# Kernel tuning notes

Measured on AMD Instinct MI355X. Metric: run time of the kernel, lower is better.

## Reference

```python
import jax, jax.numpy as jnp
import numpy as np

B, N, D = 128, 512, 512
C = D // 2
K = 4            # topk from init
NUM_SAMPLES = 500
SIGMA = 0.05
NOISE_KEY = jax.random.key(12345)


def perturbed_topk(scores):
    # scores: (B, N) -> indicators (B, K, N)
    b, d = scores.shape
    noise = jax.random.normal(NOISE_KEY, (b, NUM_SAMPLES, d), dtype=scores.dtype)
    perturbed = scores[:, None, :] + noise * SIGMA        # (B, S, N)
    _, idx = jax.lax.top_k(perturbed, K)                  # (B, S, K)
    idx = jnp.sort(idx, axis=-1)
    onehot = jax.nn.one_hot(idx, d, dtype=jnp.float32)    # (B, S, K, N)
    return onehot.mean(axis=1)                            # (B, K, N)


def layer_norm(x, w, b, eps=1e-5):
    mu = x.mean(-1, keepdims=True)
    var = ((x - mu) ** 2).mean(-1, keepdims=True)
    return (x - mu) * jax.lax.rsqrt(var + eps) * w + b


def setup_inputs() -> dict:
    key = jax.random.key(0)
    ks = jax.random.split(key, 8)
    s = lambda fan_in: 1.0 / np.sqrt(fan_in)
    return {
        "x": jax.random.normal(ks[0], (B, N, D), dtype=jnp.float32),
        "input_ids": jax.random.randint(ks[1], (B, N), 0, 30000).astype(jnp.int64),
        "attention_mask": jnp.ones((B, N), dtype=jnp.float32),
        "ln_w": jnp.ones((D,), dtype=jnp.float32),
        "ln_b": jnp.zeros((D,), dtype=jnp.float32),
        "w1": jax.random.uniform(ks[2], (D, C), minval=-s(D), maxval=s(D)),
        "b1": jax.random.uniform(ks[3], (C,), minval=-s(D), maxval=s(D)),
        "w2": jax.random.uniform(ks[4], (D, C), minval=-s(D), maxval=s(D)),
        "w3": jax.random.uniform(ks[5], (C, 1), minval=-s(C), maxval=s(C)),
    }


def reference(x, input_ids, attention_mask, ln_w, ln_b, w1, b1, w2, w3):
    b, n, d = x.shape
    # TextPredictorLG.in_conv: LayerNorm -> Linear(D, D//2) -> GELU (exact erf)
    h = jax.nn.gelu(layer_norm(x, ln_w, ln_b) @ w1 + b1, approximate=False)  # (B,N,C)
    cls_pos = jnp.argmax(input_ids, axis=-1)                                 # (B,)
    g = h[jnp.arange(b), cls_pos][:, None, :]                                # (B,1,C)
    cat = jnp.concatenate([h, jnp.broadcast_to(g, (b, n, C))], axis=-1)      # (B,N,D)
    # out_conv: Linear(D, C, no bias) -> GELU -> Linear(C, 1, no bias) -> Sigmoid
    pred_score = jax.nn.sigmoid(jax.nn.gelu(cat @ w2, approximate=False) @ w3)[..., 0]  # (B,N)
    # shift attention mask left by one, zero-pad last position
    mask_new = jnp.concatenate(
        [attention_mask[:, 1:], jnp.zeros((b, 1), dtype=attention_mask.dtype)], axis=1)
    word_score = pred_score * mask_new                                       # (B,N)
    topk_indicator = perturbed_topk(word_score)                              # (B,K,N)
    cls_x = x[jnp.arange(b), cls_pos][:, None, :]                            # (B,1,D)
    selected = jnp.einsum('bkl,bld->bkd', topk_indicator, x)                 # (B,K,D)
    return jnp.concatenate([cls_x, selected], axis=1)                        # (B,1+K,D)
```

## Files before the change

### kernel.cpp

```cpp
#include <hip/hip_runtime.h>
#include <stdint.h>

#define T_B 128
#define T_N 512
#define T_D 512
#define T_C 256
#define T_S 500
#define T_K 4

#define OFF_HP       0ull
#define OFF_W1HT     67108864ull
#define OFF_W1LT     67371008ull
#define OFF_W2HT     67633152ull
#define OFF_W2LT     67764224ull
#define OFF_ROWSTAT  67895296ull
#define OFF_U        68419584ull
#define OFF_V        68420608ull
#define OFF_GTERM    68421632ull
#define OFF_SCORE    68552704ull
#define OFF_CLSPOS   68814848ull
#define OFF_COUNTS   0ull

typedef __attribute__((ext_vector_type(8))) short bf16x8;
typedef __attribute__((ext_vector_type(4))) float f32x4;

union BF8 { uint32_t u[4]; bf16x8 v; };

__device__ __forceinline__ float gelu_exact(float z) {
  return 0.5f * z * (1.0f + erff(z * 0.70710678118654752440f));
}

__device__ __forceinline__ uint32_t rne_bf16(float f) {
  uint32_t u = __float_as_uint(f);
  return (u + 0x7FFFu + ((u >> 16) & 1u)) >> 16;
}

__device__ __forceinline__ uint2 threefry2x32(uint32_t x0, uint32_t x1) {
  const uint32_t k0 = 0u;
  const uint32_t k1 = 12345u;
  const uint32_t k2 = k0 ^ k1 ^ 0x1BD11BDAu;
  x0 += k0; x1 += k1;
#define TF_ROUND(r) { x0 += x1; x1 = (x1 << (r)) | (x1 >> (32 - (r))); x1 ^= x0; }
  TF_ROUND(13) TF_ROUND(15) TF_ROUND(26) TF_ROUND(6)
  x0 += k1; x1 += k2 + 1u;
  TF_ROUND(17) TF_ROUND(29) TF_ROUND(16) TF_ROUND(24)
  x0 += k2; x1 += k0 + 2u;
  TF_ROUND(13) TF_ROUND(15) TF_ROUND(26) TF_ROUND(6)
  x0 += k0; x1 += k1 + 3u;
  TF_ROUND(17) TF_ROUND(29) TF_ROUND(16) TF_ROUND(24)
  x0 += k1; x1 += k2 + 4u;
  TF_ROUND(13) TF_ROUND(15) TF_ROUND(26) TF_ROUND(6)
  x0 += k2; x1 += k0 + 5u;
#undef TF_ROUND
  return make_uint2(x0, x1);
}

__device__ __forceinline__ float bits_to_u(uint32_t bits) {
  float f = __uint_as_float((bits >> 9) | 0x3F800000u) - 1.0f;
  float u = f * 2.0f - 0.99999994f;
  return fmaxf(-0.99999994f, u);
}

__device__ __forceinline__ float erfinv_f(float x) {
  float w = -log1pf(-x * x);
  float p;
  if (w < 5.0f) {
    w = w - 2.5f;
    p = 2.81022636e-08f;
    p = fmaf(p, w, 3.43273939e-07f);
    p = fmaf(p, w, -3.5233877e-06f);
    p = fmaf(p, w, -4.39150654e-06f);
    p = fmaf(p, w, 0.00021858087f);
    p = fmaf(p, w, -0.00125372503f);
    p = fmaf(p, w, -0.00417768164f);
    p = fmaf(p, w, 0.246640727f);
    p = fmaf(p, w, 1.50140941f);
  } else {
    w = sqrtf(w) - 3.0f;
    p = -0.000200214257f;
    p = fmaf(p, w, 0.000100950558f);
    p = fmaf(p, w, 0.00134934322f);
    p = fmaf(p, w, -0.00367342844f);
    p = fmaf(p, w, 0.00573950773f);
    p = fmaf(p, w, -0.0076224613f);
    p = fmaf(p, w, 0.00943887047f);
    p = fmaf(p, w, 1.00167406f);
    p = fmaf(p, w, 2.83297682f);
  }
  return p * x;
}

__device__ __forceinline__ void top4_wave(float v[8], const int lane, int idx[4]) {
#pragma unroll
  for (int it = 0; it < 4; it++) {
    float bv = -INFINITY;
    int bn = 0x7FFFFFFF;
#pragma unroll
    for (int j = 0; j < 8; j++) {
      const int n = (j << 6) + lane;
      const bool better = (v[j] > bv) || ((v[j] == bv) && (n < bn));
      bv = better ? v[j] : bv;
      bn = better ? n : bn;
    }
#pragma unroll
    for (int m = 32; m >= 1; m >>= 1) {
      const float ov = __shfl_xor(bv, m);
      const int   on = __shfl_xor(bn, m);
      const bool better = (ov > bv) || ((ov == bv) && (on < bn));
      bv = better ? ov : bv;
      bn = better ? on : bn;
    }
    idx[it] = bn;
    const int jj = bn >> 6;
    const bool own = (bn & 63) == lane;
#pragma unroll
    for (int j = 0; j < 8; j++)
      if (own && j == jj) v[j] = -INFINITY;
  }
}

__device__ __forceinline__ void sort4(int a[4]) {
#define CS(x, y) { int lo = min(a[x], a[y]); int hi = max(a[x], a[y]); a[x] = lo; a[y] = hi; }
  CS(0, 1) CS(2, 3) CS(0, 2) CS(1, 3) CS(1, 2)
#undef CS
}


__global__ __launch_bounds__(256) void rowstats_kernel(const float* __restrict__ x,
                                                       float2* __restrict__ rowstat) {
  const int lane = threadIdx.x & 63;
  const int row = blockIdx.x * 4 + (threadIdx.x >> 6);
  const float* xr = x + (size_t)row * 512;
  float vals[8];
  float s = 0.0f;
#pragma unroll
  for (int j = 0; j < 8; j++) { vals[j] = xr[j * 64 + lane]; s += vals[j]; }
#pragma unroll
  for (int m = 1; m < 64; m <<= 1) s += __shfl_xor(s, m);
  const float mu = s * (1.0f / 512.0f);
  float d2 = 0.0f;
#pragma unroll
  for (int j = 0; j < 8; j++) { float d = vals[j] - mu; d2 = fmaf(d, d, d2); }
#pragma unroll
  for (int m = 1; m < 64; m <<= 1) d2 += __shfl_xor(d2, m);
  const float var = d2 * (1.0f / 512.0f);
  if (lane == 0) rowstat[row] = make_float2(mu, rsqrtf(var + 1e-5f));
}

__global__ __launch_bounds__(256) void prep_kernel(const float* __restrict__ w1,
                                                   const float* __restrict__ lnw,
                                                   const float* __restrict__ w2,
                                                   ushort* __restrict__ w1hT,
                                                   ushort* __restrict__ w1lT,
                                                   ushort* __restrict__ w2hT,
                                                   ushort* __restrict__ w2lT) {
  const int c = blockIdx.x;
  const int t = threadIdx.x;
#pragma unroll
  for (int it = 0; it < 2; it++) {
    const int d = t + it * 256;
    const float f = lnw[d] * w1[d * 256 + c];
    const uint32_t hi = rne_bf16(f);
    const float lo = f - __uint_as_float(hi << 16);
    w1hT[c * 512 + d] = (ushort)hi;
    w1lT[c * 512 + d] = (ushort)rne_bf16(lo);
  }
  {
    const float f = w2[t * 256 + c];
    const uint32_t hi = rne_bf16(f);
    const float lo = f - __uint_as_float(hi << 16);
    w2hT[c * 256 + t] = (ushort)hi;
    w2lT[c * 256 + t] = (ushort)rne_bf16(lo);
  }
}

__global__ __launch_bounds__(256) void uv_kernel(const float* __restrict__ w1,
                                                 const float* __restrict__ lnw,
                                                 const float* __restrict__ lnb,
                                                 float* __restrict__ uvec,
                                                 float* __restrict__ vvec) {
  const int c = threadIdx.x;
  float u = 0.0f, v = 0.0f;
  for (int d = 0; d < 512; d++) {
    const float w = w1[d * 256 + c];
    u = fmaf(lnw[d], w, u);
    v = fmaf(lnb[d], w, v);
  }
  uvec[c] = u;
  vvec[c] = v;
}

__global__ __launch_bounds__(64) void clspos_kernel(const int* __restrict__ ids,
                                                    const float* __restrict__ x,
                                                    int* __restrict__ cls_pos,
                                                    float* __restrict__ out) {
  const int b = blockIdx.x;
  const int lane = threadIdx.x;
  unsigned long long best = 0ull;
#pragma unroll
  for (int j = 0; j < 8; j++) {
    const int n = j * 64 + lane;
    const unsigned v = (unsigned)ids[b * 512 + n];
    const unsigned long long key = ((unsigned long long)v << 32) | (unsigned)(511 - n);
    best = key > best ? key : best;
  }
#pragma unroll
  for (int m = 1; m < 64; m <<= 1) {
    const unsigned long long o = __shfl_xor(best, m);
    best = o > best ? o : best;
  }
  const int n = 511 - (int)(best & 0xFFFFFFFFu);
  if (lane == 0) cls_pos[b] = n;
  const float* xr = x + ((size_t)b * 512 + n) * 512;
  float* orow = out + (size_t)b * 2560;
#pragma unroll
  for (int j = 0; j < 8; j++) orow[j * 64 + lane] = xr[j * 64 + lane];
}

__global__ __launch_bounds__(256, 2) void gemm1_mfma(const float* __restrict__ x,
                                                     const ushort* __restrict__ w1hT,
                                                     const ushort* __restrict__ w1lT,
                                                     const float2* __restrict__ rowstat,
                                                     const float* __restrict__ uvec,
                                                     const float* __restrict__ vvec,
                                                     const float* __restrict__ b1,
                                                     uint32_t* __restrict__ Hp) {
  const int l = threadIdx.x & 63;
  const int wid = threadIdx.x >> 6;
  const int wm = wid >> 1, wn = wid & 1;
  const int lr = l & 15;
  const int g  = l >> 4;
  const int row0 = blockIdx.x * 128;

  f32x4 acc[4][8];
#pragma unroll
  for (int mt = 0; mt < 4; mt++)
#pragma unroll
    for (int nt = 0; nt < 8; nt++) acc[mt][nt] = (f32x4)0.0f;

  const float* xb = x + (size_t)(row0 + wm * 64 + lr) * 512 + g * 8;
  const ushort* bhb = w1hT + (size_t)(wn * 128 + lr) * 512 + g * 8;
  const ushort* blb = w1lT + (size_t)(wn * 128 + lr) * 512 + g * 8;

  for (int kt = 0; kt < 16; kt++) {
    const int ko = kt * 32;
    bf16x8 ah[4], al[4];
#pragma unroll
    for (int mt = 0; mt < 4; mt++) {
      const float4 f0 = *(const float4*)(xb + (size_t)mt * 16 * 512 + ko);
      const float4 f1 = *(const float4*)(xb + (size_t)mt * 16 * 512 + ko + 4);
      float f[8] = {f0.x, f0.y, f0.z, f0.w, f1.x, f1.y, f1.z, f1.w};
      BF8 H, L;
#pragma unroll
      for (int p = 0; p < 4; p++) {
        const uint32_t u0 = __float_as_uint(f[2 * p]);
        const uint32_t u1 = __float_as_uint(f[2 * p + 1]);
        H.u[p] = (u0 >> 16) | (u1 & 0xFFFF0000u);
        const float l0 = f[2 * p]     - __uint_as_float(u0 & 0xFFFF0000u);
        const float l1 = f[2 * p + 1] - __uint_as_float(u1 & 0xFFFF0000u);
        L.u[p] = rne_bf16(l0) | (rne_bf16(l1) << 16);
      }
      ah[mt] = H.v; al[mt] = L.v;
    }
#pragma unroll
    for (int nt = 0; nt < 8; nt++) {
      const bf16x8 bh = *(const bf16x8*)(bhb + (size_t)nt * 16 * 512 + ko);
      const bf16x8 bl = *(const bf16x8*)(blb + (size_t)nt * 16 * 512 + ko);
#pragma unroll
      for (int mt = 0; mt < 4; mt++) {
        acc[mt][nt] = __builtin_amdgcn_mfma_f32_16x16x32_bf16(ah[mt], bh, acc[mt][nt], 0, 0, 0);
        acc[mt][nt] = __builtin_amdgcn_mfma_f32_16x16x32_bf16(al[mt], bh, acc[mt][nt], 0, 0, 0);
        acc[mt][nt] = __builtin_amdgcn_mfma_f32_16x16x32_bf16(ah[mt], bl, acc[mt][nt], 0, 0, 0);
      }
    }
  }

#pragma unroll
  for (int mt = 0; mt < 4; mt++) {
    const int Rb = row0 + wm * 64 + mt * 16 + g * 4;
    float2 st[4];
#pragma unroll
    for (int r = 0; r < 4; r++) st[r] = rowstat[Rb + r];
#pragma unroll
    for (int nt = 0; nt < 8; nt++) {
      const int c = wn * 128 + nt * 16 + lr;
      const float uu = uvec[c];
      const float vvb = vvec[c] + b1[c];
      uint32_t pk[4];
#pragma unroll
      for (int r = 0; r < 4; r++) {
        const float z = st[r].y * (acc[mt][nt][r] - st[r].x * uu) + vvb;
        const float gg = gelu_exact(z);
        const uint32_t ug = __float_as_uint(gg);
        const uint32_t hi = ug >> 16;
        const float lo = gg - __uint_as_float(ug & 0xFFFF0000u);
        pk[r] = hi | (rne_bf16(lo) << 16);
      }
      uint32_t* dst = Hp + (size_t)(Rb >> 2) * 1024 + c * 4;
      *(uint4*)dst = make_uint4(pk[0], pk[1], pk[2], pk[3]);
    }
  }
}

__global__ __launch_bounds__(256) void gterm_kernel(const uint32_t* __restrict__ Hp,
                                                    const float* __restrict__ W2,
                                                    const int* __restrict__ cls_pos,
                                                    float* __restrict__ gterm) {
  __shared__ float gsh[256];
  const int b = blockIdx.x;
  const int t = threadIdx.x;
  const int r = b * 512 + cls_pos[b];
  const uint32_t u = Hp[(size_t)(r >> 2) * 1024 + t * 4 + (r & 3)];
  gsh[t] = __uint_as_float((u & 0xFFFFu) << 16) + __uint_as_float(u & 0xFFFF0000u);
  __syncthreads();
  float acc = 0.0f;
  for (int j = 0; j < 256; j++) acc = fmaf(gsh[j], W2[(256 + j) * 256 + t], acc);
  gterm[b * 256 + t] = acc;
}

__global__ __launch_bounds__(256, 2) void gemm2_mfma(const uint32_t* __restrict__ Hp,
                                                     const ushort* __restrict__ w2hT,
                                                     const ushort* __restrict__ w2lT,
                                                     const float* __restrict__ gterm,
                                                     const float* __restrict__ w3,
                                                     const float* __restrict__ amask,
                                                     float* __restrict__ score) {
  __shared__ float sbuf[128][2];
  const int l = threadIdx.x & 63;
  const int wid = threadIdx.x >> 6;
  const int wm = wid >> 1, wn = wid & 1;
  const int lr = l & 15;
  const int g  = l >> 4;
  const int row0 = blockIdx.x * 128;
  const int b = row0 >> 9;

  f32x4 acc[4][8];
#pragma unroll
  for (int mt = 0; mt < 4; mt++)
#pragma unroll
    for (int nt = 0; nt < 8; nt++) acc[mt][nt] = (f32x4)0.0f;

  const uint32_t* ab = Hp + (size_t)(((row0 + wm * 64) >> 2) + (lr >> 2)) * 1024 + (lr & 3) + g * 32;
  const ushort* bhb = w2hT + (size_t)(wn * 128 + lr) * 256 + g * 8;
  const ushort* blb = w2lT + (size_t)(wn * 128 + lr) * 256 + g * 8;

  for (int kt = 0; kt < 8; kt++) {
    const int ko = kt * 32;
    bf16x8 ah[4], al[4];
#pragma unroll
    for (int mt = 0; mt < 4; mt++) {
      const uint32_t* ap = ab + (size_t)mt * 4096 + kt * 128;
      uint32_t u[8];
#pragma unroll
      for (int j = 0; j < 8; j++) u[j] = ap[j * 4];
      BF8 H, L;
#pragma unroll
      for (int p = 0; p < 4; p++) {
        H.u[p] = (u[2 * p] & 0xFFFFu) | (u[2 * p + 1] << 16);
        L.u[p] = (u[2 * p] >> 16) | (u[2 * p + 1] & 0xFFFF0000u);
      }
      ah[mt] = H.v; al[mt] = L.v;
    }
#pragma unroll
    for (int nt = 0; nt < 8; nt++) {
      const bf16x8 bh = *(const bf16x8*)(bhb + (size_t)nt * 16 * 256 + ko);
      const bf16x8 bl = *(const bf16x8*)(blb + (size_t)nt * 16 * 256 + ko);
#pragma unroll
      for (int mt = 0; mt < 4; mt++) {
        acc[mt][nt] = __builtin_amdgcn_mfma_f32_16x16x32_bf16(ah[mt], bh, acc[mt][nt], 0, 0, 0);
        acc[mt][nt] = __builtin_amdgcn_mfma_f32_16x16x32_bf16(al[mt], bh, acc[mt][nt], 0, 0, 0);
        acc[mt][nt] = __builtin_amdgcn_mfma_f32_16x16x32_bf16(ah[mt], bl, acc[mt][nt], 0, 0, 0);
      }
    }
  }

  float s[4][4];
#pragma unroll
  for (int mt = 0; mt < 4; mt++)
#pragma unroll
    for (int r = 0; r < 4; r++) s[mt][r] = 0.0f;

#pragma unroll
  for (int nt = 0; nt < 8; nt++) {
    const int c = wn * 128 + nt * 16 + lr;
    const float gt = gterm[b * 256 + c];
    const float w3v = w3[c];
#pragma unroll
    for (int mt = 0; mt < 4; mt++)
#pragma unroll
      for (int r = 0; r < 4; r++)
        s[mt][r] = fmaf(gelu_exact(acc[mt][nt][r] + gt), w3v, s[mt][r]);
  }
#pragma unroll
  for (int mt = 0; mt < 4; mt++)
#pragma unroll
    for (int r = 0; r < 4; r++) {
#pragma unroll
      for (int m = 1; m < 16; m <<= 1) s[mt][r] += __shfl_xor(s[mt][r], m);
      if (lr == 0) sbuf[wm * 64 + mt * 16 + g * 4 + r][wn] = s[mt][r];
    }
  __syncthreads();
  const int t = threadIdx.x;
  if (t < 128) {
    const float ssum = sbuf[t][0] + sbuf[t][1];
    const int R = row0 + t;
    const int n = R & 511;
    const float mk = (n < 511) ? amask[(R >> 9) * 512 + n + 1] : 0.0f;
    score[R] = mk / (1.0f + expf(-ssum));
  }
}

__global__ __launch_bounds__(256) void topk_kernel(const float* __restrict__ score,
                                                   int* __restrict__ counts) {
  const int lane = threadIdx.x & 63;
  const int wid = threadIdx.x >> 6;
  const int p = blockIdx.x * 4 + wid;
  const int b = p / 500;
  const uint32_t ibase = (uint32_t)p * 512u;
  const float* sc = score + b * 512;

  float v[8];
#pragma unroll
  for (int j = 0; j < 8; j++) {
    const int n = (j << 6) + lane;
    const uint2 o = threefry2x32(0u, ibase + (uint32_t)n);
    const uint32_t bits = o.x ^ o.y;
    const float nz = 1.41421356f * erfinv_f(bits_to_u(bits));
    v[j] = sc[n] + nz * 0.05f;
  }
  int idx[4];
  top4_wave(v, lane, idx);
  sort4(idx);
  if (lane == 0) {
    const int base = b * (T_K * T_N);
#pragma unroll
    for (int k = 0; k < 4; k++)
      atomicAdd(&counts[base + k * 512 + idx[k]], 1);
  }
}

__global__ __launch_bounds__(256) void select_kernel(const int* __restrict__ counts,
                                                     const float* __restrict__ x,
                                                     float* __restrict__ out) {
  __shared__ float cnt[4][512];
  __shared__ int list[512];
  __shared__ int nlist;
  const int b = blockIdx.x;
  const int t = threadIdx.x;
  if (t == 0) nlist = 0;
  __syncthreads();
  for (int l = t; l < 512; l += 256) {
    const int base = b * 2048 + l;
    const int c0 = counts[base];
    const int c1 = counts[base + 512];
    const int c2 = counts[base + 1024];
    const int c3 = counts[base + 1536];
    cnt[0][l] = (float)c0 * (1.0f / 500.0f);
    cnt[1][l] = (float)c1 * (1.0f / 500.0f);
    cnt[2][l] = (float)c2 * (1.0f / 500.0f);
    cnt[3][l] = (float)c3 * (1.0f / 500.0f);
    if ((c0 | c1 | c2 | c3) != 0) {
      const int pos = atomicAdd(&nlist, 1);
      list[pos] = l;
    }
  }
  __syncthreads();
  const int L = nlist;
  float a0[4] = {0.f, 0.f, 0.f, 0.f};
  float a1[4] = {0.f, 0.f, 0.f, 0.f};
  for (int e = 0; e < L; e++) {
    const int l = list[e];
    const float x0 = x[((size_t)b * 512 + l) * 512 + t];
    const float x1 = x[((size_t)b * 512 + l) * 512 + t + 256];
#pragma unroll
    for (int k = 0; k < 4; k++) {
      const float c = cnt[k][l];
      a0[k] = fmaf(c, x0, a0[k]);
      a1[k] = fmaf(c, x1, a1[k]);
    }
  }
#pragma unroll
  for (int k = 0; k < 4; k++) {
    out[(size_t)b * 2560 + (k + 1) * 512 + t] = a0[k];
    out[(size_t)b * 2560 + (k + 1) * 512 + t + 256] = a1[k];
  }
}

extern "C" void kernel_launch(void* const* d_in, const int* in_sizes, int n_in,
                              void* d_out, int out_size, void* d_ws, size_t ws_size,
                              hipStream_t stream) {
  const float* x     = (const float*)d_in[0];
  const int*   ids   = (const int*)d_in[1];
  const float* amask = (const float*)d_in[2];
  const float* lnw   = (const float*)d_in[3];
  const float* lnb   = (const float*)d_in[4];
  const float* w1    = (const float*)d_in[5];
  const float* b1    = (const float*)d_in[6];
  const float* w2    = (const float*)d_in[7];
  const float* w3    = (const float*)d_in[8];
  float* out = (float*)d_out;
  char* ws = (char*)d_ws;

  uint32_t* Hp     = (uint32_t*)(ws + OFF_HP);
  ushort*   w1hT   = (ushort*)(ws + OFF_W1HT);
  ushort*   w1lT   = (ushort*)(ws + OFF_W1LT);
  ushort*   w2hT   = (ushort*)(ws + OFF_W2HT);
  ushort*   w2lT   = (ushort*)(ws + OFF_W2LT);
  float2*   rowstat= (float2*)(ws + OFF_ROWSTAT);
  float*    uvec   = (float*)(ws + OFF_U);
  float*    vvec   = (float*)(ws + OFF_V);
  float*    gterm  = (float*)(ws + OFF_GTERM);
  float*    score  = (float*)(ws + OFF_SCORE);
  int*      clspos = (int*)(ws + OFF_CLSPOS);
  int*      counts = (int*)(ws + OFF_COUNTS);

  rowstats_kernel<<<16384, 256, 0, stream>>>(x, rowstat);
  prep_kernel<<<256, 256, 0, stream>>>(w1, lnw, w2, w1hT, w1lT, w2hT, w2lT);
  uv_kernel<<<1, 256, 0, stream>>>(w1, lnw, lnb, uvec, vvec);
  clspos_kernel<<<128, 64, 0, stream>>>(ids, x, clspos, out);
  gemm1_mfma<<<512, 256, 0, stream>>>(x, w1hT, w1lT, rowstat, uvec, vvec, b1, Hp);
  gterm_kernel<<<128, 256, 0, stream>>>(Hp, w2, clspos, gterm);
  gemm2_mfma<<<512, 256, 0, stream>>>(Hp, w2hT, w2lT, gterm, w3, amask, score);
  hipMemsetAsync(counts, 0, 128 * 4 * 512 * sizeof(int), stream);
  topk_kernel<<<16000, 256, 0, stream>>>(score, counts);
  select_kernel<<<128, 256, 0, stream>>>(counts, x, out);
}
```

Before: 681.1 us.

## Halve GEMM row tiles for more blocks and streamline noisy top-k selection

Both MFMA GEMM kernels now process 64 rows per block instead of 128, with twice as many blocks and launch bounds raised to three blocks per CU. The aim is better occupancy and load balance on a GPU with many CUs, at the cost of reloading the weight tiles more often. The top-k kernel evaluates both erfinv branches without divergence, uses a fast log2 in place of log1pf, and packs each shifted positive float with its index into a 64-bit key so each wave reduction needs one shuffle instead of two. The faster log and the different rounding order could change which samples tie or cross, which would shift the top-k counts slightly.

```diff
diff --git a/kernel.cpp b/kernel.cpp
--- a/kernel.cpp
+++ b/kernel.cpp
@@ -55,70 +55,6 @@
   return make_uint2(x0, x1);
 }
 
-__device__ __forceinline__ float bits_to_u(uint32_t bits) {
-  float f = __uint_as_float((bits >> 9) | 0x3F800000u) - 1.0f;
-  float u = f * 2.0f - 0.99999994f;
-  return fmaxf(-0.99999994f, u);
-}
-
-__device__ __forceinline__ float erfinv_f(float x) {
-  float w = -log1pf(-x * x);
-  float p;
-  if (w < 5.0f) {
-    w = w - 2.5f;
-    p = 2.81022636e-08f;
-    p = fmaf(p, w, 3.43273939e-07f);
-    p = fmaf(p, w, -3.5233877e-06f);
-    p = fmaf(p, w, -4.39150654e-06f);
-    p = fmaf(p, w, 0.00021858087f);
-    p = fmaf(p, w, -0.00125372503f);
-    p = fmaf(p, w, -0.00417768164f);
-    p = fmaf(p, w, 0.246640727f);
-    p = fmaf(p, w, 1.50140941f);
-  } else {
-    w = sqrtf(w) - 3.0f;
-    p = -0.000200214257f;
-    p = fmaf(p, w, 0.000100950558f);
-    p = fmaf(p, w, 0.00134934322f);
-    p = fmaf(p, w, -0.00367342844f);
-    p = fmaf(p, w, 0.00573950773f);
-    p = fmaf(p, w, -0.0076224613f);
-    p = fmaf(p, w, 0.00943887047f);
-    p = fmaf(p, w, 1.00167406f);
-    p = fmaf(p, w, 2.83297682f);
-  }
-  return p * x;
-}
-
-__device__ __forceinline__ void top4_wave(float v[8], const int lane, int idx[4]) {
-#pragma unroll
-  for (int it = 0; it < 4; it++) {
-    float bv = -INFINITY;
-    int bn = 0x7FFFFFFF;
-#pragma unroll
-    for (int j = 0; j < 8; j++) {
-      const int n = (j << 6) + lane;
-      const bool better = (v[j] > bv) || ((v[j] == bv) && (n < bn));
-      bv = better ? v[j] : bv;
-      bn = better ? n : bn;
-    }
-#pragma unroll
-    for (int m = 32; m >= 1; m >>= 1) {
-      const float ov = __shfl_xor(bv, m);
-      const int   on = __shfl_xor(bn, m);
-      const bool better = (ov > bv) || ((ov == bv) && (on < bn));
-      bv = better ? ov : bv;
-      bn = better ? on : bn;
-    }
-    idx[it] = bn;
-    const int jj = bn >> 6;
-    const bool own = (bn & 63) == lane;
-#pragma unroll
-    for (int j = 0; j < 8; j++)
-      if (own && j == jj) v[j] = -INFINITY;
-  }
-}
-
 __device__ __forceinline__ void sort4(int a[4]) {
 #define CS(x, y) { int lo = min(a[x], a[y]); int hi = max(a[x], a[y]); a[x] = lo; a[y] = hi; }
   CS(0, 1) CS(2, 3) CS(0, 2) CS(1, 3) CS(1, 2)
@@ -217,7 +153,7 @@
   for (int j = 0; j < 8; j++) orow[j * 64 + lane] = xr[j * 64 + lane];
 }
 
-__global__ __launch_bounds__(256, 2) void gemm1_mfma(const float* __restrict__ x,
+__global__ __launch_bounds__(256, 3) void gemm1_mfma(const float* __restrict__ x,
                                                      const ushort* __restrict__ w1hT,
                                                      const ushort* __restrict__ w1lT,
                                                      const float2* __restrict__ rowstat,
@@ -230,23 +166,23 @@
   const int wm = wid >> 1, wn = wid & 1;
   const int lr = l & 15;
   const int g  = l >> 4;
-  const int row0 = blockIdx.x * 128;
-
-  f32x4 acc[4][8];
-#pragma unroll
-  for (int mt = 0; mt < 4; mt++)
+  const int row0 = blockIdx.x * 64;
+
+  f32x4 acc[2][8];
+#pragma unroll
+  for (int mt = 0; mt < 2; mt++)
 #pragma unroll
     for (int nt = 0; nt < 8; nt++) acc[mt][nt] = (f32x4)0.0f;
 
-  const float* xb = x + (size_t)(row0 + wm * 64 + lr) * 512 + g * 8;
+  const float* xb = x + (size_t)(row0 + wm * 32 + lr) * 512 + g * 8;
   const ushort* bhb = w1hT + (size_t)(wn * 128 + lr) * 512 + g * 8;
   const ushort* blb = w1lT + (size_t)(wn * 128 + lr) * 512 + g * 8;
 
   for (int kt = 0; kt < 16; kt++) {
     const int ko = kt * 32;
-    bf16x8 ah[4], al[4];
-#pragma unroll
-    for (int mt = 0; mt < 4; mt++) {
+    bf16x8 ah[2], al[2];
+#pragma unroll
+    for (int mt = 0; mt < 2; mt++) {
       const float4 f0 = *(const float4*)(xb + (size_t)mt * 16 * 512 + ko);
       const float4 f1 = *(const float4*)(xb + (size_t)mt * 16 * 512 + ko + 4);
       float f[8] = {f0.x, f0.y, f0.z, f0.w, f1.x, f1.y, f1.z, f1.w};
@@ -267,7 +203,7 @@
       const bf16x8 bh = *(const bf16x8*)(bhb + (size_t)nt * 16 * 512 + ko);
       const bf16x8 bl = *(const bf16x8*)(blb + (size_t)nt * 16 * 512 + ko);
 #pragma unroll
-      for (int mt = 0; mt < 4; mt++) {
+      for (int mt = 0; mt < 2; mt++) {
         acc[mt][nt] = __builtin_amdgcn_mfma_f32_16x16x32_bf16(ah[mt], bh, acc[mt][nt], 0, 0, 0);
         acc[mt][nt] = __builtin_amdgcn_mfma_f32_16x16x32_bf16(al[mt], bh, acc[mt][nt], 0, 0, 0);
         acc[mt][nt] = __builtin_amdgcn_mfma_f32_16x16x32_bf16(ah[mt], bl, acc[mt][nt], 0, 0, 0);
@@ -276,8 +212,8 @@
   }
 
 #pragma unroll
-  for (int mt = 0; mt < 4; mt++) {
-    const int Rb = row0 + wm * 64 + mt * 16 + g * 4;
+  for (int mt = 0; mt < 2; mt++) {
+    const int Rb = row0 + wm * 32 + mt * 16 + g * 4;
     float2 st[4];
 #pragma unroll
     for (int r = 0; r < 4; r++) st[r] = rowstat[Rb + r];
@@ -318,37 +254,37 @@
   gterm[b * 256 + t] = acc;
 }
 
-__global__ __launch_bounds__(256, 2) void gemm2_mfma(const uint32_t* __restrict__ Hp,
+__global__ __launch_bounds__(256, 3) void gemm2_mfma(const uint32_t* __restrict__ Hp,
                                                      const ushort* __restrict__ w2hT,
                                                      const ushort* __restrict__ w2lT,
                                                      const float* __restrict__ gterm,
                                                      const float* __restrict__ w3,
                                                      const float* __restrict__ amask,
                                                      float* __restrict__ score) {
-  __shared__ float sbuf[128][2];
+  __shared__ float sbuf[64][2];
   const int l = threadIdx.x & 63;
   const int wid = threadIdx.x >> 6;
   const int wm = wid >> 1, wn = wid & 1;
   const int lr = l & 15;
   const int g  = l >> 4;
-  const int row0 = blockIdx.x * 128;
+  const int row0 = blockIdx.x * 64;
   const int b = row0 >> 9;
 
-  f32x4 acc[4][8];
-#pragma unroll
-  for (int mt = 0; mt < 4; mt++)
+  f32x4 acc[2][8];
+#pragma unroll
+  for (int mt = 0; mt < 2; mt++)
 #pragma unroll
     for (int nt = 0; nt < 8; nt++) acc[mt][nt] = (f32x4)0.0f;
 
-  const uint32_t* ab = Hp + (size_t)(((row0 + wm * 64) >> 2) + (lr >> 2)) * 1024 + (lr & 3) + g * 32;
+  const uint32_t* ab = Hp + (size_t)(((row0 + wm * 32) >> 2) + (lr >> 2)) * 1024 + (lr & 3) + g * 32;
   const ushort* bhb = w2hT + (size_t)(wn * 128 + lr) * 256 + g * 8;
   const ushort* blb = w2lT + (size_t)(wn * 128 + lr) * 256 + g * 8;
 
   for (int kt = 0; kt < 8; kt++) {
     const int ko = kt * 32;
-    bf16x8 ah[4], al[4];
-#pragma unroll
-    for (int mt = 0; mt < 4; mt++) {
+    bf16x8 ah[2], al[2];
+#pragma unroll
+    for (int mt = 0; mt < 2; mt++) {
       const uint32_t* ap = ab + (size_t)mt * 4096 + kt * 128;
       uint32_t u[8];
 #pragma unroll
@@ -366,7 +302,7 @@
       const bf16x8 bh = *(const bf16x8*)(bhb + (size_t)nt * 16 * 256 + ko);
       const bf16x8 bl = *(const bf16x8*)(blb + (size_t)nt * 16 * 256 + ko);
 #pragma unroll
-      for (int mt = 0; mt < 4; mt++) {
+      for (int mt = 0; mt < 2; mt++) {
         acc[mt][nt] = __builtin_amdgcn_mfma_f32_16x16x32_bf16(ah[mt], bh, acc[mt][nt], 0, 0, 0);
         acc[mt][nt] = __builtin_amdgcn_mfma_f32_16x16x32_bf16(al[mt], bh, acc[mt][nt], 0, 0, 0);
         acc[mt][nt] = __builtin_amdgcn_mfma_f32_16x16x32_bf16(ah[mt], bl, acc[mt][nt], 0, 0, 0);
@@ -374,9 +310,9 @@
     }
   }
 
-  float s[4][4];
-#pragma unroll
-  for (int mt = 0; mt < 4; mt++)
+  float s[2][4];
+#pragma unroll
+  for (int mt = 0; mt < 2; mt++)
 #pragma unroll
     for (int r = 0; r < 4; r++) s[mt][r] = 0.0f;
 
@@ -386,22 +322,22 @@
     const float gt = gterm[b * 256 + c];
     const float w3v = w3[c];
 #pragma unroll
-    for (int mt = 0; mt < 4; mt++)
+    for (int mt = 0; mt < 2; mt++)
 #pragma unroll
       for (int r = 0; r < 4; r++)
         s[mt][r] = fmaf(gelu_exact(acc[mt][nt][r] + gt), w3v, s[mt][r]);
   }
 #pragma unroll
-  for (int mt = 0; mt < 4; mt++)
+  for (int mt = 0; mt < 2; mt++)
 #pragma unroll
     for (int r = 0; r < 4; r++) {
 #pragma unroll
       for (int m = 1; m < 16; m <<= 1) s[mt][r] += __shfl_xor(s[mt][r], m);
-      if (lr == 0) sbuf[wm * 64 + mt * 16 + g * 4 + r][wn] = s[mt][r];
+      if (lr == 0) sbuf[wm * 32 + mt * 16 + g * 4 + r][wn] = s[mt][r];
     }
   __syncthreads();
   const int t = threadIdx.x;
-  if (t < 128) {
+  if (t < 64) {
     const float ssum = sbuf[t][0] + sbuf[t][1];
     const int R = row0 + t;
     const int n = R & 511;
@@ -419,23 +355,72 @@
   const uint32_t ibase = (uint32_t)p * 512u;
   const float* sc = score + b * 512;
 
-  float v[8];
+  uint32_t hi[8];
 #pragma unroll
   for (int j = 0; j < 8; j++) {
     const int n = (j << 6) + lane;
     const uint2 o = threefry2x32(0u, ibase + (uint32_t)n);
     const uint32_t bits = o.x ^ o.y;
-    const float nz = 1.41421356f * erfinv_f(bits_to_u(bits));
-    v[j] = sc[n] + nz * 0.05f;
-  }
-  int idx[4];
-  top4_wave(v, lane, idx);
-  sort4(idx);
+    const float f = __uint_as_float((bits >> 9) | 0x3F800000u) - 1.0f;
+    const float x = fmaxf(-0.99999994f, fmaf(f, 2.0f, -0.99999994f));
+    const float t = fmaf(-x, x, 1.0f);
+    const float w = -0.69314718056f * __log2f(t);
+    const float wa = w - 2.5f;
+    const float wb = sqrtf(w) - 3.0f;
+    float pa = 2.81022636e-08f;
+    pa = fmaf(pa, wa, 3.43273939e-07f);
+    pa = fmaf(pa, wa, -3.5233877e-06f);
+    pa = fmaf(pa, wa, -4.39150654e-06f);
+    pa = fmaf(pa, wa, 0.00021858087f);
+    pa = fmaf(pa, wa, -0.00125372503f);
+    pa = fmaf(pa, wa, -0.00417768164f);
+    pa = fmaf(pa, wa, 0.246640727f);
+    pa = fmaf(pa, wa, 1.50140941f);
+    float pb = -0.000200214257f;
+    pb = fmaf(pb, wb, 0.000100950558f);
+    pb = fmaf(pb, wb, 0.00134934322f);
+    pb = fmaf(pb, wb, -0.00367342844f);
+    pb = fmaf(pb, wb, 0.00573950773f);
+    pb = fmaf(pb, wb, -0.0076224613f);
+    pb = fmaf(pb, wb, 0.00943887047f);
+    pb = fmaf(pb, wb, 1.00167406f);
+    pb = fmaf(pb, wb, 2.83297682f);
+    const float pp = (w < 5.0f) ? pa : pb;
+    const float val = fmaf(pp * x, 0.07071067812f, sc[n]);
+    hi[j] = __float_as_uint(val + 1.0f);
+  }
+
+  int res[4];
+#pragma unroll
+  for (int it = 0; it < 4; it++) {
+    uint32_t bh = hi[0];
+    int bl = 511 - lane;
+#pragma unroll
+    for (int j = 1; j < 8; j++) {
+      const int loj = 511 - ((j << 6) + lane);
+      if (hi[j] > bh) { bh = hi[j]; bl = loj; }
+    }
+    unsigned long long k = ((unsigned long long)bh << 32) | (unsigned)bl;
+#pragma unroll
+    for (int m = 32; m >= 1; m >>= 1) {
+      const unsigned long long ok = __shfl_xor(k, m);
+      k = ok > k ? ok : k;
+    }
+    const int bn = 511 - (int)(k & 0xFFFFu);
+    res[it] = bn;
+    if ((bn & 63) == lane) {
+      const int jj = bn >> 6;
+#pragma unroll
+      for (int j = 0; j < 8; j++)
+        if (j == jj) hi[j] = 0u;
+    }
+  }
+  sort4(res);
   if (lane == 0) {
     const int base = b * (T_K * T_N);
 #pragma unroll
-    for (int k = 0; k < 4; k++)
-      atomicAdd(&counts[base + k * 512 + idx[k]], 1);
+    for (int kk = 0; kk < 4; kk++)
+      atomicAdd(&counts[base + kk * 512 + res[kk]], 1);
   }
 }
 
@@ -518,9 +503,9 @@
   prep_kernel<<<256, 256, 0, stream>>>(w1, lnw, w2, w1hT, w1lT, w2hT, w2lT);
   uv_kernel<<<1, 256, 0, stream>>>(w1, lnw, lnb, uvec, vvec);
   clspos_kernel<<<128, 64, 0, stream>>>(ids, x, clspos, out);
-  gemm1_mfma<<<512, 256, 0, stream>>>(x, w1hT, w1lT, rowstat, uvec, vvec, b1, Hp);
+  gemm1_mfma<<<1024, 256, 0, stream>>>(x, w1hT, w1lT, rowstat, uvec, vvec, b1, Hp);
   gterm_kernel<<<128, 256, 0, stream>>>(Hp, w2, clspos, gterm);
-  gemm2_mfma<<<512, 256, 0, stream>>>(Hp, w2hT, w2lT, gterm, w3, amask, score);
+  gemm2_mfma<<<1024, 256, 0, stream>>>(Hp, w2hT, w2lT, gterm, w3, amask, score);
   hipMemsetAsync(counts, 0, 128 * 4 * 512 * sizeof(int), stream);
   topk_kernel<<<16000, 256, 0, stream>>>(score, counts);
   select_kernel<<<128, 256, 0, stream>>>(counts, x, out);
```

Result: no change. 668.6 us (-1.8%).
